# Kernel tuning notes

Hardware: AMD Instinct MI355X
Metric: run time of the kernel (lower is better)

Reference implementation:

```python
import jax, jax.numpy as jnp
import numpy as np

B, M = 512, 2048            # batch of src-tgt pairs, sampled walk positions per pair
NUM_KEYS = 1_000_000        # unique (node, time) keys in nodetime2emb map
NUM_NODES = 100_000
LP = 4                      # num_layers + 1 (saw encoding width)
ENC = 32                    # enc_dim
FEAT = 64                   # node feature dim (MergeLayer dim2)
D3, D4 = 64, 1              # MergeLayer hidden / output dims


def setup_inputs() -> dict:
    key = jax.random.key(0)
    ks = jax.random.split(key, 12)
    s = 0.05
    return {
        "pos_table": jax.random.uniform(ks[0], (NUM_KEYS, LP), dtype=jnp.float32),
        "node_feat": jax.random.normal(ks[1], (NUM_NODES, FEAT), dtype=jnp.float32),
        "W1": jax.random.normal(ks[2], (LP, ENC), dtype=jnp.float32) * s,
        "b1": jnp.zeros((ENC,), dtype=jnp.float32),
        "W2": jax.random.normal(ks[3], (ENC, ENC), dtype=jnp.float32) * s,
        "b2": jnp.zeros((ENC,), dtype=jnp.float32),
        "Wm1": jax.random.normal(ks[4], (ENC + FEAT, D3), dtype=jnp.float32) * s,
        "bm1": jnp.zeros((D3,), dtype=jnp.float32),
        "Wm2": jax.random.normal(ks[5], (D3, D4), dtype=jnp.float32) * s,
        "bm2": jnp.zeros((D4,), dtype=jnp.float32),
        "key_idx": jax.random.randint(ks[6], (B, M), 0, NUM_KEYS, dtype=jnp.int32),
        "node_idx": jax.random.randint(ks[7], (B, M), 0, NUM_NODES, dtype=jnp.int32),
    }


def reference(pos_table, node_feat, W1, b1, W2, b2, Wm1, bm1, Wm2, bm2, key_idx, node_idx):
    # PositionEncoder.forward: gather saw encodings by (node, time) key,
    # then trainable_embedding = Linear(LP->ENC) -> ReLU -> Linear(ENC->ENC)
    enc = pos_table[key_idx]                       # [B, M, LP] irregular gather
    pe = jax.nn.relu(enc @ W1 + b1) @ W2 + b2      # [B, M, ENC]
    # gather raw node features for the same walk positions
    feat = node_feat[node_idx]                     # [B, M, FEAT] irregular gather
    # MergeLayer (non_linear=True): concat -> fc1 -> ReLU -> fc2
    x = jnp.concatenate([pe, feat], axis=-1)       # [B, M, ENC+FEAT]
    z = jax.nn.relu(x @ Wm1 + bm1) @ Wm2 + bm2     # [B, M, 1]
    return z
```

## Files before the change

### kernel.cpp

```cpp
#include <hip/hip_runtime.h>


typedef _Float16 half8 __attribute__((ext_vector_type(8)));
typedef float floatx4 __attribute__((ext_vector_type(4)));

#define HSTR 40
#define WSTR 104
#define GRID_MAIN 1024

__global__ void feat_to_f16(const float* __restrict__ nf,
                            _Float16* __restrict__ o, int n8) {
    int t = blockIdx.x * 256 + threadIdx.x;
    if (t >= n8) return;
    const float4* p = (const float4*)nf + (size_t)t * 2;
    const float4 a = p[0], b = p[1];
    half8 h;
    h[0] = (_Float16)a.x; h[1] = (_Float16)a.y;
    h[2] = (_Float16)a.z; h[3] = (_Float16)a.w;
    h[4] = (_Float16)b.x; h[5] = (_Float16)b.y;
    h[6] = (_Float16)b.z; h[7] = (_Float16)b.w;
    *((half8*)o + t) = h;
}

__global__ __launch_bounds__(256, 3) void neurtw_r12(
    const float* __restrict__ pos_table,
    const float* __restrict__ node_feat,
    const float* __restrict__ W1,
    const float* __restrict__ b1,
    const float* __restrict__ W2,
    const float* __restrict__ b2,
    const float* __restrict__ Wm1,
    const float* __restrict__ bm1,
    const float* __restrict__ Wm2,
    const float* __restrict__ bm2,
    const int*   __restrict__ key_idx,
    const int*   __restrict__ node_idx,
    const _Float16* __restrict__ feat16,
    int use_f16,
    float*       __restrict__ out,
    int rows)
{
    __shared__ _Float16 hpe[256 * HSTR];
    __shared__ _Float16 wm1t[64 * WSTR];

    const int tid  = threadIdx.x;
    const int lane = tid & 63;
    const int r0   = (tid >> 6) * 64;
    const int ln   = lane & 15;
    const int q    = lane >> 4;

    #pragma unroll
    for (int i = 0; i < 3; ++i) {
        const int task = i * 256 + tid;
        const int n = task & 63, k8 = task >> 6;
        half8 w;
        #pragma unroll
        for (int kk = 0; kk < 8; ++kk)
            w[kk] = (_Float16)Wm1[(k8 * 8 + kk) * 64 + n];
        *(half8*)(&wm1t[n * WSTR + k8 * 8]) = w;
    }

    half8 b_w2[2];
    #pragma unroll
    for (int ct = 0; ct < 2; ++ct)
        #pragma unroll
        for (int j = 0; j < 8; ++j)
            b_w2[ct][j] = (_Float16)W2[(q * 8 + j) * 32 + ct * 16 + ln];
    float b2v[2];
    b2v[0] = b2[ln]; b2v[1] = b2[16 + ln];
    float bm1v[4], wm2v[4];
    #pragma unroll
    for (int ct = 0; ct < 4; ++ct) {
        bm1v[ct] = bm1[ct * 16 + ln];
        wm2v[ct] = Wm2[ct * 16 + ln];
    }
    const float bm2s = bm2[0];

    __syncthreads();

    for (int base = blockIdx.x * 256; base < rows; base += GRID_MAIN * 256) {
        const int row = base + tid;

        int ndr[4];
        #pragma unroll
        for (int rt = 0; rt < 4; ++rt)
            ndr[rt] = node_idx[base + r0 + rt * 16 + ln];

        half8 fA[4][2];
        if (use_f16) {
            #pragma unroll
            for (int rt = 0; rt < 4; ++rt) {
                const _Float16* fb = feat16 + (size_t)ndr[rt] * 64 + q * 8;
                fA[rt][0] = *(const half8*)(fb);
                fA[rt][1] = *(const half8*)(fb + 32);
            }
        } else {
            #pragma unroll
            for (int rt = 0; rt < 4; ++rt) {
                const float* fb = node_feat + (size_t)ndr[rt] * 64 + q * 8;
                #pragma unroll
                for (int kt = 0; kt < 2; ++kt) {
                    const float4 lo = *(const float4*)(fb + kt * 32);
                    const float4 hi = *(const float4*)(fb + kt * 32 + 4);
                    half8 h;
                    h[0] = (_Float16)lo.x; h[1] = (_Float16)lo.y;
                    h[2] = (_Float16)lo.z; h[3] = (_Float16)lo.w;
                    h[4] = (_Float16)hi.x; h[5] = (_Float16)hi.y;
                    h[6] = (_Float16)hi.z; h[7] = (_Float16)hi.w;
                    fA[rt][kt] = h;
                }
            }
        }

        const int kk = key_idx[row];
        const float4 enc = *(const float4*)(pos_table + (size_t)kk * 4);

        #pragma unroll
        for (int g = 0; g < 4; ++g) {
            half8 hv;
            #pragma unroll
            for (int j8 = 0; j8 < 8; ++j8) {
                const int j = g * 8 + j8;
                float a = fmaf(enc.w, W1[96 + j],
                          fmaf(enc.z, W1[64 + j],
                          fmaf(enc.y, W1[32 + j],
                          fmaf(enc.x, W1[j], b1[j]))));
                hv[j8] = (_Float16)fmaxf(a, 0.0f);
            }
            *(half8*)(&hpe[tid * HSTR + g * 8]) = hv;
        }
        half8 a_h[4];
        #pragma unroll
        for (int rt = 0; rt < 4; ++rt)
            a_h[rt] = *(const half8*)(&hpe[(r0 + rt * 16 + ln) * HSTR + q * 8]);

        floatx4 pc[4][2];
        #pragma unroll
        for (int rt = 0; rt < 4; ++rt)
            #pragma unroll
            for (int ct = 0; ct < 2; ++ct) {
                floatx4 c = {0.f, 0.f, 0.f, 0.f};
                pc[rt][ct] = __builtin_amdgcn_mfma_f32_16x16x32_f16(
                    a_h[rt], b_w2[ct], c, 0, 0, 0);
            }

        #pragma unroll
        for (int rt = 0; rt < 4; ++rt)
            #pragma unroll
            for (int ct = 0; ct < 2; ++ct)
                #pragma unroll
                for (int r = 0; r < 4; ++r)
                    hpe[(r0 + rt * 16 + q * 4 + r) * HSTR + ct * 16 + ln] =
                        (_Float16)(pc[rt][ct][r] + b2v[ct]);

        floatx4 acc[4][4];
        #pragma unroll
        for (int ct = 0; ct < 4; ++ct) {
            const float bb = bm1v[ct];
            #pragma unroll
            for (int rt = 0; rt < 4; ++rt)
                acc[rt][ct] = (floatx4){bb, bb, bb, bb};
        }

        {
            half8 a_pe[4];
            #pragma unroll
            for (int rt = 0; rt < 4; ++rt)
                a_pe[rt] = *(const half8*)(&hpe[(r0 + rt * 16 + ln) * HSTR + q * 8]);
            half8 b0[4];
            #pragma unroll
            for (int ct = 0; ct < 4; ++ct)
                b0[ct] = *(const half8*)(&wm1t[(ct * 16 + ln) * WSTR + q * 8]);
            #pragma unroll
            for (int rt = 0; rt < 4; ++rt)
                #pragma unroll
                for (int ct = 0; ct < 4; ++ct)
                    acc[rt][ct] = __builtin_amdgcn_mfma_f32_16x16x32_f16(
                        a_pe[rt], b0[ct], acc[rt][ct], 0, 0, 0);
        }

        #pragma unroll
        for (int kt = 0; kt < 2; ++kt) {
            half8 bk[4];
            #pragma unroll
            for (int ct = 0; ct < 4; ++ct)
                bk[ct] = *(const half8*)(&wm1t[(ct * 16 + ln) * WSTR + 32 + kt * 32 + q * 8]);
            #pragma unroll
            for (int rt = 0; rt < 4; ++rt)
                #pragma unroll
                for (int ct = 0; ct < 4; ++ct)
                    acc[rt][ct] = __builtin_amdgcn_mfma_f32_16x16x32_f16(
                        fA[rt][kt], bk[ct], acc[rt][ct], 0, 0, 0);
        }

        #pragma unroll
        for (int rt = 0; rt < 4; ++rt) {
            #pragma unroll
            for (int r = 0; r < 4; ++r) {
                float p = 0.0f;
                #pragma unroll
                for (int ct = 0; ct < 4; ++ct)
                    p = fmaf(fmaxf(acc[rt][ct][r], 0.0f), wm2v[ct], p);
                p += __shfl_xor(p, 1);
                p += __shfl_xor(p, 2);
                p += __shfl_xor(p, 4);
                p += __shfl_xor(p, 8);
                if (ln == 0)
                    out[base + r0 + rt * 16 + q * 4 + r] = p + bm2s;
            }
        }
    }
}

extern "C" void kernel_launch(void* const* d_in, const int* in_sizes, int n_in,
                              void* d_out, int out_size, void* d_ws, size_t ws_size,
                              hipStream_t stream) {
    const float* pos_table = (const float*)d_in[0];
    const float* node_feat = (const float*)d_in[1];
    const float* W1        = (const float*)d_in[2];
    const float* b1        = (const float*)d_in[3];
    const float* W2        = (const float*)d_in[4];
    const float* b2        = (const float*)d_in[5];
    const float* Wm1       = (const float*)d_in[6];
    const float* bm1       = (const float*)d_in[7];
    const float* Wm2       = (const float*)d_in[8];
    const float* bm2       = (const float*)d_in[9];
    const int*   key_idx   = (const int*)d_in[10];
    const int*   node_idx  = (const int*)d_in[11];
    float* out = (float*)d_out;

    const int rows  = in_sizes[10];
    const int nfeat = in_sizes[1];

    _Float16* feat16 = (_Float16*)d_ws;
    const size_t need = (size_t)nfeat * sizeof(_Float16);
    const int use_f16 = (ws_size >= need) ? 1 : 0;

    if (use_f16) {
        const int n8 = nfeat / 8;
        feat_to_f16<<<(n8 + 255) / 256, 256, 0, stream>>>(node_feat, feat16, n8);
    }

    neurtw_r12<<<GRID_MAIN, 256, 0, stream>>>(
        pos_table, node_feat, W1, b1, W2, b2, Wm1, bm1, Wm2, bm2,
        key_idx, node_idx, feat16, use_f16, out, rows);
}
```

Measured before the change: 173.0 us.

## Cut register pressure to raise occupancy by moving constants to LDS and splitting feature gathers

Raises the launch-bounds occupancy target from 3 to 4 waves per SIMD. To fit that register budget, the W2 fragments, b2, bm1 and Wm2 values that each thread used to hold in registers are now stored in shared memory and reloaded where needed, with an opaque zero offset so the compiler cannot hoist those loads back out. The node-feature gather is also split in two: rows 0-1 are loaded first and fed into MFMAs, and rows 2-3 are loaded later, shortening the lifetime of the gathered fragments. The trade-off is extra LDS reads per iteration and less overlap of gather latency, in exchange for more resident waves to hide memory latency.

Result: no change. 175.2 us (+1.3%).

```diff
diff --git a/kernel.cpp b/kernel.cpp
--- a/kernel.cpp
+++ b/kernel.cpp
@@ -22,7 +22,7 @@
     *((half8*)o + t) = h;
 }
 
-__global__ __launch_bounds__(256, 3) void neurtw_r12(
+__global__ __launch_bounds__(256, 4) void neurtw_r13(
     const float* __restrict__ pos_table,
     const float* __restrict__ node_feat,
     const float* __restrict__ W1,
@@ -42,6 +42,10 @@
 {
     __shared__ _Float16 hpe[256 * HSTR];
     __shared__ _Float16 wm1t[64 * WSTR];
+    __shared__ _Float16 cw2[2 * 64 * 8];
+    __shared__ float    cb2[32];
+    __shared__ float    cbm1[64];
+    __shared__ float    cwm2[64];
 
     const int tid  = threadIdx.x;
     const int lane = tid & 63;
@@ -60,19 +64,20 @@
         *(half8*)(&wm1t[n * WSTR + k8 * 8]) = w;
     }
 
-    half8 b_w2[2];
-    #pragma unroll
-    for (int ct = 0; ct < 2; ++ct)
+    if (tid < 128) {
+        const int ct = tid >> 6, l = tid & 63;
+        const int lq = l >> 4, lln = l & 15;
+        half8 w;
         #pragma unroll
         for (int j = 0; j < 8; ++j)
-            b_w2[ct][j] = (_Float16)W2[(q * 8 + j) * 32 + ct * 16 + ln];
-    float b2v[2];
-    b2v[0] = b2[ln]; b2v[1] = b2[16 + ln];
-    float bm1v[4], wm2v[4];
-    #pragma unroll
-    for (int ct = 0; ct < 4; ++ct) {
-        bm1v[ct] = bm1[ct * 16 + ln];
-        wm2v[ct] = Wm2[ct * 16 + ln];
+            w[j] = (_Float16)W2[(lq * 8 + j) * 32 + ct * 16 + lln];
+        *(half8*)(&cw2[ct * 512 + l * 8]) = w;
+    }
+    if (tid < 32) cb2[tid] = b2[tid];
+    if (tid >= 128 && tid < 192) {
+        const int t = tid - 128;
+        cbm1[t] = bm1[t];
+        cwm2[t] = Wm2[t];
     }
     const float bm2s = bm2[0];
 
@@ -81,22 +86,25 @@
     for (int base = blockIdx.x * 256; base < rows; base += GRID_MAIN * 256) {
         const int row = base + tid;
 
+        int oz = 0;
+        asm volatile("" : "+v"(oz));
+
         int ndr[4];
         #pragma unroll
         for (int rt = 0; rt < 4; ++rt)
             ndr[rt] = node_idx[base + r0 + rt * 16 + ln];
 
-        half8 fA[4][2];
+        half8 fA01[2][2];
         if (use_f16) {
             #pragma unroll
-            for (int rt = 0; rt < 4; ++rt) {
+            for (int rt = 0; rt < 2; ++rt) {
                 const _Float16* fb = feat16 + (size_t)ndr[rt] * 64 + q * 8;
-                fA[rt][0] = *(const half8*)(fb);
-                fA[rt][1] = *(const half8*)(fb + 32);
+                fA01[rt][0] = *(const half8*)(fb);
+                fA01[rt][1] = *(const half8*)(fb + 32);
             }
         } else {
             #pragma unroll
-            for (int rt = 0; rt < 4; ++rt) {
+            for (int rt = 0; rt < 2; ++rt) {
                 const float* fb = node_feat + (size_t)ndr[rt] * 64 + q * 8;
                 #pragma unroll
                 for (int kt = 0; kt < 2; ++kt) {
@@ -107,7 +115,7 @@
                     h[2] = (_Float16)lo.z; h[3] = (_Float16)lo.w;
                     h[4] = (_Float16)hi.x; h[5] = (_Float16)hi.y;
                     h[6] = (_Float16)hi.z; h[7] = (_Float16)hi.w;
-                    fA[rt][kt] = h;
+                    fA01[rt][kt] = h;
                 }
             }
         }
@@ -134,49 +142,84 @@
         for (int rt = 0; rt < 4; ++rt)
             a_h[rt] = *(const half8*)(&hpe[(r0 + rt * 16 + ln) * HSTR + q * 8]);
 
-        floatx4 pc[4][2];
-        #pragma unroll
-        for (int rt = 0; rt < 4; ++rt)
-            #pragma unroll
-            for (int ct = 0; ct < 2; ++ct) {
+        #pragma unroll
+        for (int ct = 0; ct < 2; ++ct) {
+            const half8 bw2 = *(const half8*)(&cw2[ct * 512 + lane * 8 + oz]);
+            const float vb2 = cb2[ct * 16 + ln + oz];
+            #pragma unroll
+            for (int rt = 0; rt < 4; ++rt) {
                 floatx4 c = {0.f, 0.f, 0.f, 0.f};
-                pc[rt][ct] = __builtin_amdgcn_mfma_f32_16x16x32_f16(
-                    a_h[rt], b_w2[ct], c, 0, 0, 0);
-            }
-
-        #pragma unroll
-        for (int rt = 0; rt < 4; ++rt)
-            #pragma unroll
-            for (int ct = 0; ct < 2; ++ct)
+                floatx4 pcv = __builtin_amdgcn_mfma_f32_16x16x32_f16(
+                    a_h[rt], bw2, c, 0, 0, 0);
                 #pragma unroll
                 for (int r = 0; r < 4; ++r)
                     hpe[(r0 + rt * 16 + q * 4 + r) * HSTR + ct * 16 + ln] =
-                        (_Float16)(pc[rt][ct][r] + b2v[ct]);
+                        (_Float16)(pcv[r] + vb2);
+            }
+        }
 
         floatx4 acc[4][4];
         #pragma unroll
         for (int ct = 0; ct < 4; ++ct) {
-            const float bb = bm1v[ct];
+            const float bb = cbm1[ct * 16 + ln + oz];
             #pragma unroll
             for (int rt = 0; rt < 4; ++rt)
                 acc[rt][ct] = (floatx4){bb, bb, bb, bb};
         }
 
+        #pragma unroll
+        for (int kt = 0; kt < 2; ++kt) {
+            half8 bk[4];
+            #pragma unroll
+            for (int ct = 0; ct < 4; ++ct)
+                bk[ct] = *(const half8*)(&wm1t[(ct * 16 + ln) * WSTR + 32 + kt * 32 + q * 8]);
+            #pragma unroll
+            for (int rt = 0; rt < 2; ++rt)
+                #pragma unroll
+                for (int ct = 0; ct < 4; ++ct)
+                    acc[rt][ct] = __builtin_amdgcn_mfma_f32_16x16x32_f16(
+                        fA01[rt][kt], bk[ct], acc[rt][ct], 0, 0, 0);
+        }
+
+        half8 fA23[2][2];
+        if (use_f16) {
+            #pragma unroll
+            for (int rr = 0; rr < 2; ++rr) {
+                const _Float16* fb = feat16 + (size_t)ndr[2 + rr] * 64 + q * 8;
+                fA23[rr][0] = *(const half8*)(fb);
+                fA23[rr][1] = *(const half8*)(fb + 32);
+            }
+        } else {
+            #pragma unroll
+            for (int rr = 0; rr < 2; ++rr) {
+                const float* fb = node_feat + (size_t)ndr[2 + rr] * 64 + q * 8;
+                #pragma unroll
+                for (int kt = 0; kt < 2; ++kt) {
+                    const float4 lo = *(const float4*)(fb + kt * 32);
+                    const float4 hi = *(const float4*)(fb + kt * 32 + 4);
+                    half8 h;
+                    h[0] = (_Float16)lo.x; h[1] = (_Float16)lo.y;
+                    h[2] = (_Float16)lo.z; h[3] = (_Float16)lo.w;
+                    h[4] = (_Float16)hi.x; h[5] = (_Float16)hi.y;
+                    h[6] = (_Float16)hi.z; h[7] = (_Float16)hi.w;
+                    fA23[rr][kt] = h;
+                }
+            }
+        }
+
         {
-            half8 a_pe[4];
-            #pragma unroll
-            for (int rt = 0; rt < 4; ++rt)
-                a_pe[rt] = *(const half8*)(&hpe[(r0 + rt * 16 + ln) * HSTR + q * 8]);
             half8 b0[4];
             #pragma unroll
             for (int ct = 0; ct < 4; ++ct)
                 b0[ct] = *(const half8*)(&wm1t[(ct * 16 + ln) * WSTR + q * 8]);
             #pragma unroll
-            for (int rt = 0; rt < 4; ++rt)
+            for (int rt = 0; rt < 4; ++rt) {
+                const half8 ap = *(const half8*)(&hpe[(r0 + rt * 16 + ln) * HSTR + q * 8]);
                 #pragma unroll
                 for (int ct = 0; ct < 4; ++ct)
                     acc[rt][ct] = __builtin_amdgcn_mfma_f32_16x16x32_f16(
-                        a_pe[rt], b0[ct], acc[rt][ct], 0, 0, 0);
+                        ap, b0[ct], acc[rt][ct], 0, 0, 0);
+            }
         }
 
         #pragma unroll
@@ -186,12 +229,17 @@
             for (int ct = 0; ct < 4; ++ct)
                 bk[ct] = *(const half8*)(&wm1t[(ct * 16 + ln) * WSTR + 32 + kt * 32 + q * 8]);
             #pragma unroll
-            for (int rt = 0; rt < 4; ++rt)
-                #pragma unroll
-                for (int ct = 0; ct < 4; ++ct)
-                    acc[rt][ct] = __builtin_amdgcn_mfma_f32_16x16x32_f16(
-                        fA[rt][kt], bk[ct], acc[rt][ct], 0, 0, 0);
-        }
+            for (int rr = 0; rr < 2; ++rr)
+                #pragma unroll
+                for (int ct = 0; ct < 4; ++ct)
+                    acc[2 + rr][ct] = __builtin_amdgcn_mfma_f32_16x16x32_f16(
+                        fA23[rr][kt], bk[ct], acc[2 + rr][ct], 0, 0, 0);
+        }
+
+        float wv[4];
+        #pragma unroll
+        for (int ct = 0; ct < 4; ++ct)
+            wv[ct] = cwm2[ct * 16 + ln + oz];
 
         #pragma unroll
         for (int rt = 0; rt < 4; ++rt) {
@@ -200,7 +248,7 @@
                 float p = 0.0f;
                 #pragma unroll
                 for (int ct = 0; ct < 4; ++ct)
-                    p = fmaf(fmaxf(acc[rt][ct][r], 0.0f), wm2v[ct], p);
+                    p = fmaf(fmaxf(acc[rt][ct][r], 0.0f), wv[ct], p);
                 p += __shfl_xor(p, 1);
                 p += __shfl_xor(p, 2);
                 p += __shfl_xor(p, 4);
@@ -241,7 +289,7 @@
         feat_to_f16<<<(n8 + 255) / 256, 256, 0, stream>>>(node_feat, feat16, n8);
     }
 
-    neurtw_r12<<<GRID_MAIN, 256, 0, stream>>>(
+    neurtw_r13<<<GRID_MAIN, 256, 0, stream>>>(
         pos_table, node_feat, W1, b1, W2, b2, Wm1, bm1, Wm2, bm2,
         key_idx, node_idx, feat16, use_f16, out, rows);
 }
```

## Software-pipeline gathers across iterations with smaller per-block row tiles

Applied to the files above, without the earlier changes.

Cuts each block's tile from 256 to 128 rows, so each wave handles 32 rows with two row-tiles, and raises the launch-bounds occupancy hint from 3 to 4 blocks. The node-index, key-index, pos_table and first feature-tile gathers for the next iteration are issued during the current iteration's compute, so gather latency overlaps with the MFMA work. The first-layer embedding compute is split across lane halves, 32 rows by 16 columns each. The cost is more loop iterations and more live registers for the prefetched values, which could limit the occupancy the new hint targets.

After: 310.3 us. 79.4% more time.

```diff
diff --git a/kernel.cpp b/kernel.cpp
--- a/kernel.cpp
+++ b/kernel.cpp
@@ -7,6 +7,7 @@
 #define HSTR 40
 #define WSTR 104
 #define GRID_MAIN 1024
+#define IT_ROWS (GRID_MAIN * 128)
 
 __global__ void feat_to_f16(const float* __restrict__ nf,
                             _Float16* __restrict__ o, int n8) {
@@ -22,7 +23,31 @@
     *((half8*)o + t) = h;
 }
 
-__global__ __launch_bounds__(256, 3) void neurtw_r12(
+__device__ __forceinline__ void load_feat1(const _Float16* __restrict__ feat16,
+                                           const float* __restrict__ node_feat,
+                                           int use_f16, int nd, int q,
+                                           half8 fA[2]) {
+    if (use_f16) {
+        const _Float16* fb = feat16 + (size_t)nd * 64 + q * 8;
+        fA[0] = *(const half8*)(fb);
+        fA[1] = *(const half8*)(fb + 32);
+    } else {
+        const float* fb = node_feat + (size_t)nd * 64 + q * 8;
+        #pragma unroll
+        for (int kt = 0; kt < 2; ++kt) {
+            const float4 lo = *(const float4*)(fb + kt * 32);
+            const float4 hi = *(const float4*)(fb + kt * 32 + 4);
+            half8 h;
+            h[0] = (_Float16)lo.x; h[1] = (_Float16)lo.y;
+            h[2] = (_Float16)lo.z; h[3] = (_Float16)lo.w;
+            h[4] = (_Float16)hi.x; h[5] = (_Float16)hi.y;
+            h[6] = (_Float16)hi.z; h[7] = (_Float16)hi.w;
+            fA[kt] = h;
+        }
+    }
+}
+
+__global__ __launch_bounds__(256, 4) void neurtw_r21(
     const float* __restrict__ pos_table,
     const float* __restrict__ node_feat,
     const float* __restrict__ W1,
@@ -40,14 +65,16 @@
     float*       __restrict__ out,
     int rows)
 {
-    __shared__ _Float16 hpe[256 * HSTR];
+    __shared__ _Float16 hpe[128 * HSTR];
     __shared__ _Float16 wm1t[64 * WSTR];
 
     const int tid  = threadIdx.x;
     const int lane = tid & 63;
-    const int r0   = (tid >> 6) * 64;
+    const int wr0  = (tid >> 6) * 32;
     const int ln   = lane & 15;
     const int q    = lane >> 4;
+    const int rloc = lane & 31;
+    const int jh   = lane >> 5;
 
     #pragma unroll
     for (int i = 0; i < 3; ++i) {
@@ -78,65 +105,58 @@
 
     __syncthreads();
 
-    for (int base = blockIdx.x * 256; base < rows; base += GRID_MAIN * 256) {
-        const int row = base + tid;
-
-        int ndr[4];
-        #pragma unroll
-        for (int rt = 0; rt < 4; ++rt)
-            ndr[rt] = node_idx[base + r0 + rt * 16 + ln];
-
-        half8 fA[4][2];
-        if (use_f16) {
-            #pragma unroll
-            for (int rt = 0; rt < 4; ++rt) {
-                const _Float16* fb = feat16 + (size_t)ndr[rt] * 64 + q * 8;
-                fA[rt][0] = *(const half8*)(fb);
-                fA[rt][1] = *(const half8*)(fb + 32);
-            }
+    int base = blockIdx.x * 128;
+    int ndr[2];
+    #pragma unroll
+    for (int rt = 0; rt < 2; ++rt)
+        ndr[rt] = node_idx[base + wr0 + rt * 16 + ln];
+    int kkc = key_idx[base + wr0 + rloc];
+    float4 enc = *(const float4*)(pos_table + (size_t)kkc * 4);
+    half8 fA0[2];
+    load_feat1(feat16, node_feat, use_f16, ndr[0], q, fA0);
+
+    while (base < rows) {
+        const int nbase = base + IT_ROWS;
+        const bool more = nbase < rows;
+
+        half8 fA1[2];
+        load_feat1(feat16, node_feat, use_f16, ndr[1], q, fA1);
+
+        int ndr_n[2];
+        int kk_n;
+        if (more) {
+            #pragma unroll
+            for (int rt = 0; rt < 2; ++rt)
+                ndr_n[rt] = node_idx[nbase + wr0 + rt * 16 + ln];
+            kk_n = key_idx[nbase + wr0 + rloc];
         } else {
-            #pragma unroll
-            for (int rt = 0; rt < 4; ++rt) {
-                const float* fb = node_feat + (size_t)ndr[rt] * 64 + q * 8;
-                #pragma unroll
-                for (int kt = 0; kt < 2; ++kt) {
-                    const float4 lo = *(const float4*)(fb + kt * 32);
-                    const float4 hi = *(const float4*)(fb + kt * 32 + 4);
-                    half8 h;
-                    h[0] = (_Float16)lo.x; h[1] = (_Float16)lo.y;
-                    h[2] = (_Float16)lo.z; h[3] = (_Float16)lo.w;
-                    h[4] = (_Float16)hi.x; h[5] = (_Float16)hi.y;
-                    h[6] = (_Float16)hi.z; h[7] = (_Float16)hi.w;
-                    fA[rt][kt] = h;
-                }
-            }
-        }
-
-        const int kk = key_idx[row];
-        const float4 enc = *(const float4*)(pos_table + (size_t)kk * 4);
-
-        #pragma unroll
-        for (int g = 0; g < 4; ++g) {
+            ndr_n[0] = 0; ndr_n[1] = 0;
+            kk_n = 0;
+        }
+
+        const int hrow = wr0 + rloc;
+        #pragma unroll
+        for (int g = 0; g < 2; ++g) {
             half8 hv;
             #pragma unroll
             for (int j8 = 0; j8 < 8; ++j8) {
-                const int j = g * 8 + j8;
+                const int j = jh * 16 + g * 8 + j8;
                 float a = fmaf(enc.w, W1[96 + j],
                           fmaf(enc.z, W1[64 + j],
                           fmaf(enc.y, W1[32 + j],
                           fmaf(enc.x, W1[j], b1[j]))));
                 hv[j8] = (_Float16)fmaxf(a, 0.0f);
             }
-            *(half8*)(&hpe[tid * HSTR + g * 8]) = hv;
-        }
-        half8 a_h[4];
-        #pragma unroll
-        for (int rt = 0; rt < 4; ++rt)
-            a_h[rt] = *(const half8*)(&hpe[(r0 + rt * 16 + ln) * HSTR + q * 8]);
-
-        floatx4 pc[4][2];
-        #pragma unroll
-        for (int rt = 0; rt < 4; ++rt)
+            *(half8*)(&hpe[hrow * HSTR + jh * 16 + g * 8]) = hv;
+        }
+        half8 a_h[2];
+        #pragma unroll
+        for (int rt = 0; rt < 2; ++rt)
+            a_h[rt] = *(const half8*)(&hpe[(wr0 + rt * 16 + ln) * HSTR + q * 8]);
+
+        floatx4 pc[2][2];
+        #pragma unroll
+        for (int rt = 0; rt < 2; ++rt)
             #pragma unroll
             for (int ct = 0; ct < 2; ++ct) {
                 floatx4 c = {0.f, 0.f, 0.f, 0.f};
@@ -145,34 +165,37 @@
             }
 
         #pragma unroll
-        for (int rt = 0; rt < 4; ++rt)
+        for (int rt = 0; rt < 2; ++rt)
             #pragma unroll
             for (int ct = 0; ct < 2; ++ct)
                 #pragma unroll
                 for (int r = 0; r < 4; ++r)
-                    hpe[(r0 + rt * 16 + q * 4 + r) * HSTR + ct * 16 + ln] =
+                    hpe[(wr0 + rt * 16 + q * 4 + r) * HSTR + ct * 16 + ln] =
                         (_Float16)(pc[rt][ct][r] + b2v[ct]);
 
-        floatx4 acc[4][4];
+        float4 enc_n = enc;
+        if (more)
+            enc_n = *(const float4*)(pos_table + (size_t)kk_n * 4);
+
+        floatx4 acc[2][4];
         #pragma unroll
         for (int ct = 0; ct < 4; ++ct) {
             const float bb = bm1v[ct];
-            #pragma unroll
-            for (int rt = 0; rt < 4; ++rt)
-                acc[rt][ct] = (floatx4){bb, bb, bb, bb};
+            acc[0][ct] = (floatx4){bb, bb, bb, bb};
+            acc[1][ct] = (floatx4){bb, bb, bb, bb};
         }
 
         {
-            half8 a_pe[4];
-            #pragma unroll
-            for (int rt = 0; rt < 4; ++rt)
-                a_pe[rt] = *(const half8*)(&hpe[(r0 + rt * 16 + ln) * HSTR + q * 8]);
+            half8 a_pe[2];
+            #pragma unroll
+            for (int rt = 0; rt < 2; ++rt)
+                a_pe[rt] = *(const half8*)(&hpe[(wr0 + rt * 16 + ln) * HSTR + q * 8]);
             half8 b0[4];
             #pragma unroll
             for (int ct = 0; ct < 4; ++ct)
                 b0[ct] = *(const half8*)(&wm1t[(ct * 16 + ln) * WSTR + q * 8]);
             #pragma unroll
-            for (int rt = 0; rt < 4; ++rt)
+            for (int rt = 0; rt < 2; ++rt)
                 #pragma unroll
                 for (int ct = 0; ct < 4; ++ct)
                     acc[rt][ct] = __builtin_amdgcn_mfma_f32_16x16x32_f16(
@@ -186,15 +209,19 @@
             for (int ct = 0; ct < 4; ++ct)
                 bk[ct] = *(const half8*)(&wm1t[(ct * 16 + ln) * WSTR + 32 + kt * 32 + q * 8]);
             #pragma unroll
-            for (int rt = 0; rt < 4; ++rt)
-                #pragma unroll
-                for (int ct = 0; ct < 4; ++ct)
-                    acc[rt][ct] = __builtin_amdgcn_mfma_f32_16x16x32_f16(
-                        fA[rt][kt], bk[ct], acc[rt][ct], 0, 0, 0);
-        }
-
-        #pragma unroll
-        for (int rt = 0; rt < 4; ++rt) {
+            for (int ct = 0; ct < 4; ++ct) {
+                acc[0][ct] = __builtin_amdgcn_mfma_f32_16x16x32_f16(
+                    fA0[kt], bk[ct], acc[0][ct], 0, 0, 0);
+                acc[1][ct] = __builtin_amdgcn_mfma_f32_16x16x32_f16(
+                    fA1[kt], bk[ct], acc[1][ct], 0, 0, 0);
+            }
+        }
+
+        half8 fA0_n[2];
+        load_feat1(feat16, node_feat, use_f16, ndr_n[0], q, fA0_n);
+
+        #pragma unroll
+        for (int rt = 0; rt < 2; ++rt) {
             #pragma unroll
             for (int r = 0; r < 4; ++r) {
                 float p = 0.0f;
@@ -206,9 +233,17 @@
                 p += __shfl_xor(p, 4);
                 p += __shfl_xor(p, 8);
                 if (ln == 0)
-                    out[base + r0 + rt * 16 + q * 4 + r] = p + bm2s;
-            }
-        }
+                    out[base + wr0 + rt * 16 + q * 4 + r] = p + bm2s;
+            }
+        }
+
+        base = nbase;
+        ndr[0] = ndr_n[0];
+        ndr[1] = ndr_n[1];
+        kkc = kk_n;
+        enc = enc_n;
+        fA0[0] = fA0_n[0];
+        fA0[1] = fA0_n[1];
     }
 }
 
@@ -241,7 +276,7 @@
         feat_to_f16<<<(n8 + 255) / 256, 256, 0, stream>>>(node_feat, feat16, n8);
     }
 
-    neurtw_r12<<<GRID_MAIN, 256, 0, stream>>>(
+    neurtw_r21<<<GRID_MAIN, 256, 0, stream>>>(
         pos_table, node_feat, W1, b1, W2, b2, Wm1, bm1, Wm2, bm2,
         key_idx, node_idx, feat16, use_f16, out, rows);
 }
```
